# Kernel optimization log

Measured on AMD Instinct MI355X. Metric: run time of the kernel, lower is better.

Reference implementation:

```python
import jax, jax.numpy as jnp
import numpy as np

B, N_PER, N_TOOL, D, T = 64, 4096, 1000, 128, 50
SCALE = 50.0  # self.scale_pcl_val


def setup_inputs() -> dict:
    key = jax.random.key(0)
    ks = jax.random.split(key, 9)
    return {
        "x_feat": jax.random.normal(ks[0], (B * N_PER, D), jnp.float32),
        "pos": jax.random.normal(ks[1], (B * N_PER, 3), jnp.float32),
        "tool_idx": jax.random.randint(ks[2], (B, N_TOOL), 0, N_PER, jnp.int32),
        "W1": jax.random.normal(ks[3], (D, D), jnp.float32) * 0.05,
        "b1": jnp.zeros((D,), jnp.float32),
        "W2": jax.random.normal(ks[4], (D, D), jnp.float32) * 0.05,
        "b2": jnp.zeros((D,), jnp.float32),
        "W3": jax.random.normal(ks[5], (D, 3 * T), jnp.float32) * 0.05,
        "b3": jnp.zeros((3 * T,), jnp.float32),
    }


def _kabsch(xyz, flow):
    # xyz, flow: [B, N, 3]; fit rigid transform mapping xyz -> xyz + flow (Kabsch/SVD)
    y = xyz + flow
    mu_x = xyz.mean(axis=1, keepdims=True)
    mu_y = y.mean(axis=1, keepdims=True)
    xc = xyz - mu_x
    yc = y - mu_y
    H = jnp.einsum('bni,bnj->bij', xc, yc)  # [B,3,3] covariance
    U, S, Vt = jnp.linalg.svd(H)
    d = jnp.sign(jnp.linalg.det(U @ Vt))  # reflection fix, [B]
    Dm = jnp.stack([jnp.ones_like(d), jnp.ones_like(d), d], axis=-1)  # [B,3]
    R = (U * Dm[:, None, :]) @ Vt  # [B,3,3]
    return jnp.einsum('bni,bij->bnj', xc, R) + mu_y  # transformed points


def reference(x_feat, pos, tool_idx, W1, b1, W2, b2, W3, b3):
    # MLP([128,128,128,flow_dim]) head (eval mode: dropout off)
    h = jax.nn.relu(x_feat @ W1 + b1)
    h = jax.nn.relu(h @ W2 + b2)
    flow_per_pt = (h @ W3 + b3).reshape(B, N_PER, T, 3)

    pos_s = (pos * SCALE).reshape(B, N_PER, 3)  # data['pos'] * scale_pcl_val
    idx3 = tool_idx[:, :, None]
    xyz0 = jnp.take_along_axis(pos_s, idx3, axis=1)  # [B, N_TOOL, 3]
    flows = jnp.take_along_axis(flow_per_pt, tool_idx[:, :, None, None], axis=1)  # [B, N_TOOL, T, 3]
    flows_t = jnp.moveaxis(flows, 2, 0)  # [T, B, N_TOOL, 3]

    def step(xyz, flow):
        new_xyz = _kabsch(xyz, flow)
        return new_xyz, (new_xyz - xyz, flow)

    _, (flow_traj, before_svd) = jax.lax.scan(step, xyz0, flows_t)
    flow_traj = jnp.moveaxis(flow_traj, 0, 1)      # [B, T, N_TOOL, 3]
    before_svd = jnp.moveaxis(before_svd, 0, 1)    # [B, T, N_TOOL, 3]
    return flow_traj, before_svd
```

## Files before the change

kernel.cpp:

```cpp
#include <hip/hip_runtime.h>
#include <cstddef>

#define HB 64
#define HN_PER 4096
#define HN_TOOL 1000
#define HD 128
#define HT 50
#define HSCALE 50.0f

typedef _Float16 f16x8 __attribute__((ext_vector_type(8)));
typedef float f32x4 __attribute__((ext_vector_type(4)));

constexpr int TILE_M = 64;
constexpr int NBLK1 = (HB * HN_TOOL) / TILE_M;
constexpr int APITCH = 136;

constexpr int W1_BASE = 0;
constexpr int W2_BASE = 16384;
constexpr int W3_BASE = 32768;

constexpr int XC0_F = 26624;
constexpr int C0_F  = XC0_F + HB * HN_TOOL * 3;
constexpr int BT_F  = C0_F + HB * 9;
constexpr int MT_F  = BT_F + HB * HT * 12;

__global__ __launch_bounds__(256) void wconv_kernel(
    const float* __restrict__ W1, const float* __restrict__ W2,
    const float* __restrict__ W3, _Float16* __restrict__ ws)
{
    const int gid = blockIdx.x * 256 + threadIdx.x;
    const int lane = gid & 63, f = gid >> 6;
    const float* W; int ncols, base, fi;
    if (f < 32)       { W = W1; ncols = 128; base = W1_BASE; fi = f; }
    else if (f < 64)  { W = W2; ncols = 128; base = W2_BASE; fi = f - 32; }
    else if (f < 104) { W = W3; ncols = 150; base = W3_BASE; fi = f - 64; }
    else return;
    const int nt = fi >> 2, kc = fi & 3;
    const int col = nt * 16 + (lane & 15);
    const int k0 = kc * 32 + (lane >> 4) * 8;
    f16x8 v;
#pragma unroll
    for (int j = 0; j < 8; ++j)
        v[j] = (col < ncols) ? (_Float16)W[(size_t)(k0 + j) * ncols + col]
                             : (_Float16)0.f;
    *(f16x8*)(ws + ((size_t)(base + (fi * 64 + lane) * 8))) = v;
}

__device__ __forceinline__ float wave_red_sum(float v)
{
#define DPP_ADD(ctrl)                                                          \
    v += __builtin_bit_cast(float, __builtin_amdgcn_update_dpp(                \
             0, __builtin_bit_cast(int, v), (ctrl), 0xF, 0xF, true));
    DPP_ADD(0x128)
    DPP_ADD(0x124)
    DPP_ADD(0x122)
    DPP_ADD(0x121)
#undef DPP_ADD
    v += __shfl_xor(v, 16, 64);
    v += __shfl_xor(v, 32, 64);
    return v;
}

__global__ __launch_bounds__(256) void init_kernel(
    const float* __restrict__ pos,
    const int* __restrict__ tool_idx,
    float* __restrict__ ws)
{
    __shared__ float red[4][6];
    const int b = blockIdx.x;
    const int tid = threadIdx.x;
    const int lane = tid & 63, wv = tid >> 6;

    float px[4], py[4], pz[4];
    int cnt = 0;
#pragma unroll
    for (int s = 0; s < 4; ++s) {
        const int n = tid + 256 * s;
        if (n < HN_TOOL) {
            const int p = tool_idx[b * HN_TOOL + n];
            const float* pp = pos + (size_t)(b * HN_PER + p) * 3;
            px[s] = pp[0] * HSCALE;
            py[s] = pp[1] * HSCALE;
            pz[s] = pp[2] * HSCALE;
            cnt = s + 1;
        }
    }
    float s0 = 0.f, s1 = 0.f, s2 = 0.f;
    for (int s = 0; s < cnt; ++s) { s0 += px[s]; s1 += py[s]; s2 += pz[s]; }
    s0 = wave_red_sum(s0); s1 = wave_red_sum(s1); s2 = wave_red_sum(s2);
    if (lane == 0) { red[wv][0] = s0; red[wv][1] = s1; red[wv][2] = s2; }
    __syncthreads();
    const float invN = 1.0f / HN_TOOL;
    const float mux = (red[0][0] + red[1][0] + red[2][0] + red[3][0]) * invN;
    const float muy = (red[0][1] + red[1][1] + red[2][1] + red[3][1]) * invN;
    const float muz = (red[0][2] + red[1][2] + red[2][2] + red[3][2]) * invN;
    __syncthreads();

    float xx = 0.f, xy = 0.f, xz = 0.f, yy = 0.f, yz = 0.f, zz = 0.f;
    float* xc = ws + XC0_F + (size_t)b * HN_TOOL * 3;
    for (int s = 0; s < cnt; ++s) {
        const int n = tid + 256 * s;
        const float x = px[s] - mux, y = py[s] - muy, z = pz[s] - muz;
        xc[3 * n + 0] = x; xc[3 * n + 1] = y; xc[3 * n + 2] = z;
        xx += x * x; xy += x * y; xz += x * z;
        yy += y * y; yz += y * z; zz += z * z;
    }
    float c6[6] = {xx, xy, xz, yy, yz, zz};
#pragma unroll
    for (int v = 0; v < 6; ++v) c6[v] = wave_red_sum(c6[v]);
    if (lane == 0) {
#pragma unroll
        for (int v = 0; v < 6; ++v) red[wv][v] = c6[v];
    }
    __syncthreads();
    if (tid == 0) {
        float g[6];
#pragma unroll
        for (int v = 0; v < 6; ++v)
            g[v] = red[0][v] + red[1][v] + red[2][v] + red[3][v];
        float* c0 = ws + C0_F + b * 9;
        c0[0] = g[0]; c0[1] = g[1]; c0[2] = g[2];
        c0[3] = g[1]; c0[4] = g[3]; c0[5] = g[4];
        c0[6] = g[2]; c0[7] = g[4]; c0[8] = g[5];
    }
}

__global__ __launch_bounds__(256) void mlp_mfma_kernel(
    const float* __restrict__ x_feat,
    const int* __restrict__ tool_idx,
    const _Float16* __restrict__ Wsw,
    const float* __restrict__ b1, const float* __restrict__ b2,
    const float* __restrict__ b3,
    float* __restrict__ out2)
{
    __shared__ __align__(16) _Float16 hA[TILE_M][APITCH];
    const int tid = threadIdx.x;
    const int lane = tid & 63, w = tid >> 6;
    const int lm = lane & 15, quad = lane >> 4;
    const int m0 = w * 16;

    {
        const int i = tid >> 2;
        const int c0 = (tid & 3) * 32;
        const int r = blockIdx.x * TILE_M + i;
        const int b = r / HN_TOOL;
        const int n = r - b * HN_TOOL;
        const int p = tool_idx[b * HN_TOOL + n];
        const float4* src =
            (const float4*)(x_feat + (size_t)(b * HN_PER + p) * HD + c0);
#pragma unroll
        for (int fq = 0; fq < 4; ++fq) {
            const float4 u = src[2 * fq], v = src[2 * fq + 1];
            f16x8 h = {(_Float16)u.x, (_Float16)u.y, (_Float16)u.z, (_Float16)u.w,
                       (_Float16)v.x, (_Float16)v.y, (_Float16)v.z, (_Float16)v.w};
            *(f16x8*)&hA[i][c0 + fq * 8] = h;
        }
    }
    __syncthreads();

#pragma unroll
    for (int layer = 0; layer < 2; ++layer) {
        const _Float16* wb = Wsw + (layer ? W2_BASE : W1_BASE);
        const float* bias = layer ? b2 : b1;
        f16x8 afr[4];
#pragma unroll
        for (int kc = 0; kc < 4; ++kc)
            afr[kc] = *(const f16x8*)&hA[m0 + lm][kc * 32 + quad * 8];
        f32x4 acc[8];
#pragma unroll
        for (int nt = 0; nt < 8; ++nt) acc[nt] = (f32x4){0.f, 0.f, 0.f, 0.f};
#pragma unroll
        for (int kc = 0; kc < 4; ++kc)
#pragma unroll
            for (int nt = 0; nt < 8; ++nt) {
                const f16x8 bf = *(const f16x8*)(wb + (size_t)((nt * 4 + kc) * 64 + lane) * 8);
                acc[nt] = __builtin_amdgcn_mfma_f32_16x16x32_f16(afr[kc], bf, acc[nt], 0, 0, 0);
            }
#pragma unroll
        for (int nt = 0; nt < 8; ++nt) {
            const float bb = bias[nt * 16 + lm];
#pragma unroll
            for (int r = 0; r < 4; ++r)
                hA[m0 + quad * 4 + r][nt * 16 + lm] =
                    (_Float16)fmaxf(acc[nt][r] + bb, 0.f);
        }
    }

    {
        f16x8 afr[4];
#pragma unroll
        for (int kc = 0; kc < 4; ++kc)
            afr[kc] = *(const f16x8*)&hA[m0 + lm][kc * 32 + quad * 8];
        f32x4 acc[10];
#pragma unroll
        for (int nt = 0; nt < 10; ++nt) acc[nt] = (f32x4){0.f, 0.f, 0.f, 0.f};
#pragma unroll
        for (int kc = 0; kc < 4; ++kc)
#pragma unroll
            for (int nt = 0; nt < 10; ++nt) {
                const f16x8 bf = *(const f16x8*)(Wsw + W3_BASE + (size_t)((nt * 4 + kc) * 64 + lane) * 8);
                acc[nt] = __builtin_amdgcn_mfma_f32_16x16x32_f16(afr[kc], bf, acc[nt], 0, 0, 0);
            }
#pragma unroll
        for (int nt = 0; nt < 10; ++nt) {
            const int j = nt * 16 + lm;
            if (j < 150) {
                const float bb = b3[j];
                const int t = j / 3, c = j - 3 * t;
#pragma unroll
                for (int r = 0; r < 4; ++r) {
                    const int gr = blockIdx.x * TILE_M + m0 + quad * 4 + r;
                    const int b = gr / HN_TOOL;
                    const int n = gr - b * HN_TOOL;
                    out2[(size_t)b * HT * HN_TOOL * 3 +
                         ((size_t)t * HN_TOOL + n) * 3 + c] = acc[nt][r] + bb;
                }
            }
        }
    }
}

__global__ __launch_bounds__(256) void mom_kernel(
    const float* __restrict__ flows,
    float* __restrict__ ws)
{
    __shared__ float red[4][12];
    const int t = blockIdx.x, b = blockIdx.y;
    const int tid = threadIdx.x;
    const int lane = tid & 63, wv = tid >> 6;

    const float* xc = ws + XC0_F + (size_t)b * HN_TOOL * 3;
    const float* f = flows + ((size_t)(b * HT + t) * HN_TOOL) * 3;

    float S[12];
#pragma unroll
    for (int v = 0; v < 12; ++v) S[v] = 0.f;
#pragma unroll
    for (int s = 0; s < 4; ++s) {
        const int n = tid + 256 * s;
        if (n < HN_TOOL) {
            const float x = xc[3 * n + 0], y = xc[3 * n + 1], z = xc[3 * n + 2];
            const float fx = f[3 * n + 0], fy = f[3 * n + 1], fz = f[3 * n + 2];
            S[0] += x * fx; S[1] += x * fy; S[2] += x * fz;
            S[3] += y * fx; S[4] += y * fy; S[5] += y * fz;
            S[6] += z * fx; S[7] += z * fy; S[8] += z * fz;
            S[9] += fx; S[10] += fy; S[11] += fz;
        }
    }
#pragma unroll
    for (int v = 0; v < 12; ++v) S[v] = wave_red_sum(S[v]);
    if (lane == 0) {
#pragma unroll
        for (int v = 0; v < 12; ++v) red[wv][v] = S[v];
    }
    __syncthreads();
    if (tid < 12)
        ws[BT_F + (size_t)(b * HT + t) * 12 + tid] =
            red[0][tid] + red[1][tid] + red[2][tid] + red[3][tid];
}

__global__ __launch_bounds__(64) void compose_kernel(float* __restrict__ ws)
{
    const int b = threadIdx.x;
    float C0[9], P[9];
#pragma unroll
    for (int v = 0; v < 9; ++v) C0[v] = ws[C0_F + b * 9 + v];
    P[0] = 1.f; P[1] = 0.f; P[2] = 0.f;
    P[3] = 0.f; P[4] = 1.f; P[5] = 0.f;
    P[6] = 0.f; P[7] = 0.f; P[8] = 1.f;

    const float invN = 1.0f / HN_TOOL;
    const float* bt = ws + BT_F + (size_t)b * HT * 12;
    float* mt = ws + MT_F + (size_t)b * HT * 12;

    float4 n0 = *(const float4*)(bt);
    float4 n1 = *(const float4*)(bt + 4);
    float4 n2 = *(const float4*)(bt + 8);

    for (int t = 0; t < HT; ++t) {
        const float Bv[12] = {n0.x, n0.y, n0.z, n0.w, n1.x, n1.y, n1.z, n1.w,
                              n2.x, n2.y, n2.z, n2.w};
        if (t + 1 < HT) {
            const float* nb = bt + (t + 1) * 12;
            n0 = *(const float4*)(nb);
            n1 = *(const float4*)(nb + 4);
            n2 = *(const float4*)(nb + 8);
        }
        float G[9];
#pragma unroll
        for (int i = 0; i < 3; ++i)
#pragma unroll
            for (int j = 0; j < 3; ++j)
                G[i * 3 + j] = C0[i * 3 + 0] * P[0 * 3 + j] +
                               C0[i * 3 + 1] * P[1 * 3 + j] +
                               C0[i * 3 + 2] * P[2 * 3 + j] + Bv[i * 3 + j];
        float X[9];
#pragma unroll
        for (int i = 0; i < 3; ++i)
#pragma unroll
            for (int j = 0; j < 3; ++j)
                X[i * 3 + j] = P[0 * 3 + i] * G[0 * 3 + j] +
                               P[1 * 3 + i] * G[1 * 3 + j] +
                               P[2 * 3 + i] * G[2 * 3 + j];
        const float scl = 3.0f / (X[0] + X[4] + X[8]);
#pragma unroll
        for (int v = 0; v < 9; ++v) X[v] *= scl;
#pragma unroll
        for (int it = 0; it < 2; ++it) {
            float C[9];
            C[0] =  (X[4] * X[8] - X[5] * X[7]);
            C[1] = -(X[3] * X[8] - X[5] * X[6]);
            C[2] =  (X[3] * X[7] - X[4] * X[6]);
            C[3] = -(X[1] * X[8] - X[2] * X[7]);
            C[4] =  (X[0] * X[8] - X[2] * X[6]);
            C[5] = -(X[0] * X[7] - X[1] * X[6]);
            C[6] =  (X[1] * X[5] - X[2] * X[4]);
            C[7] = -(X[0] * X[5] - X[2] * X[3]);
            C[8] =  (X[0] * X[4] - X[1] * X[3]);
            const float det = X[0] * C[0] + X[1] * C[1] + X[2] * C[2];
            const float rdet = 0.5f / det;
#pragma unroll
            for (int v = 0; v < 9; ++v) X[v] = 0.5f * X[v] + C[v] * rdet;
        }
        float Pn[9];
#pragma unroll
        for (int i = 0; i < 3; ++i)
#pragma unroll
            for (int j = 0; j < 3; ++j)
                Pn[i * 3 + j] = P[i * 3 + 0] * X[0 * 3 + j] +
                                P[i * 3 + 1] * X[1 * 3 + j] +
                                P[i * 3 + 2] * X[2 * 3 + j];
        float4 m0, m1, m2;
        m0.x = Pn[0] - P[0]; m0.y = Pn[1] - P[1]; m0.z = Pn[2] - P[2];
        m0.w = Pn[3] - P[3]; m1.x = Pn[4] - P[4]; m1.y = Pn[5] - P[5];
        m1.z = Pn[6] - P[6]; m1.w = Pn[7] - P[7]; m2.x = Pn[8] - P[8];
        m2.y = Bv[9] * invN; m2.z = Bv[10] * invN; m2.w = Bv[11] * invN;
        float* mo = mt + t * 12;
        *(float4*)(mo) = m0;
        *(float4*)(mo + 4) = m1;
        *(float4*)(mo + 8) = m2;
#pragma unroll
        for (int v = 0; v < 9; ++v) P[v] = Pn[v];
    }
}

__global__ __launch_bounds__(256) void apply_kernel(
    const float* __restrict__ ws, float* __restrict__ out1)
{
    __shared__ float M[12];
    const int t = blockIdx.x, b = blockIdx.y;
    const int tid = threadIdx.x;
    if (tid < 12) M[tid] = ws[MT_F + (size_t)(b * HT + t) * 12 + tid];
    __syncthreads();

    const float* xc = ws + XC0_F + (size_t)b * HN_TOOL * 3;
    float* ot = out1 + ((size_t)(b * HT + t) * HN_TOOL) * 3;
#pragma unroll
    for (int s = 0; s < 4; ++s) {
        const int n = tid + 256 * s;
        if (n < HN_TOOL) {
            const float x = xc[3 * n + 0], y = xc[3 * n + 1], z = xc[3 * n + 2];
            ot[3 * n + 0] = x * M[0] + y * M[3] + z * M[6] + M[9];
            ot[3 * n + 1] = x * M[1] + y * M[4] + z * M[7] + M[10];
            ot[3 * n + 2] = x * M[2] + y * M[5] + z * M[8] + M[11];
        }
    }
}

extern "C" void kernel_launch(void* const* d_in, const int* in_sizes, int n_in,
                              void* d_out, int out_size, void* d_ws, size_t ws_size,
                              hipStream_t stream)
{
    const float* x_feat   = (const float*)d_in[0];
    const float* pos      = (const float*)d_in[1];
    const int*   tool_idx = (const int*)d_in[2];
    const float* W1 = (const float*)d_in[3];
    const float* b1 = (const float*)d_in[4];
    const float* W2 = (const float*)d_in[5];
    const float* b2 = (const float*)d_in[6];
    const float* W3 = (const float*)d_in[7];
    const float* b3 = (const float*)d_in[8];

    float* out1 = (float*)d_out;
    float* out2 = out1 + (size_t)HB * HT * HN_TOOL * 3;
    _Float16* wsw = (_Float16*)d_ws;
    float* wsf = (float*)d_ws;

    wconv_kernel<<<26, 256, 0, stream>>>(W1, W2, W3, wsw);
    init_kernel<<<HB, 256, 0, stream>>>(pos, tool_idx, wsf);
    mlp_mfma_kernel<<<NBLK1, 256, 0, stream>>>(
        x_feat, tool_idx, wsw, b1, b2, b3, out2);
    mom_kernel<<<dim3(HT, HB), 256, 0, stream>>>(out2, wsf);
    compose_kernel<<<1, 64, 0, stream>>>(wsf);
    apply_kernel<<<dim3(HT, HB), 256, 0, stream>>>(wsf, out1);
}
```

Baseline: 298.2 us.

## Fuse moment reduction into MLP epilogue and merge prep kernels

```diff
diff --git a/kernel.cpp b/kernel.cpp
--- a/kernel.cpp
+++ b/kernel.cpp
@@ -12,8 +12,8 @@
 typedef float f32x4 __attribute__((ext_vector_type(4)));
 
 constexpr int TILE_M = 64;
-constexpr int NBLK1 = (HB * HN_TOOL) / TILE_M;
 constexpr int APITCH = 136;
+constexpr int SPITCH = 204;
 
 constexpr int W1_BASE = 0;
 constexpr int W2_BASE = 16384;
@@ -23,28 +23,6 @@
 constexpr int C0_F  = XC0_F + HB * HN_TOOL * 3;
 constexpr int BT_F  = C0_F + HB * 9;
 constexpr int MT_F  = BT_F + HB * HT * 12;
-
-__global__ __launch_bounds__(256) void wconv_kernel(
-    const float* __restrict__ W1, const float* __restrict__ W2,
-    const float* __restrict__ W3, _Float16* __restrict__ ws)
-{
-    const int gid = blockIdx.x * 256 + threadIdx.x;
-    const int lane = gid & 63, f = gid >> 6;
-    const float* W; int ncols, base, fi;
-    if (f < 32)       { W = W1; ncols = 128; base = W1_BASE; fi = f; }
-    else if (f < 64)  { W = W2; ncols = 128; base = W2_BASE; fi = f - 32; }
-    else if (f < 104) { W = W3; ncols = 150; base = W3_BASE; fi = f - 64; }
-    else return;
-    const int nt = fi >> 2, kc = fi & 3;
-    const int col = nt * 16 + (lane & 15);
-    const int k0 = kc * 32 + (lane >> 4) * 8;
-    f16x8 v;
-#pragma unroll
-    for (int j = 0; j < 8; ++j)
-        v[j] = (col < ncols) ? (_Float16)W[(size_t)(k0 + j) * ncols + col]
-                             : (_Float16)0.f;
-    *(f16x8*)(ws + ((size_t)(base + (fi * 64 + lane) * 8))) = v;
-}
 
 __device__ __forceinline__ float wave_red_sum(float v)
 {
@@ -61,67 +39,102 @@
     return v;
 }
 
-__global__ __launch_bounds__(256) void init_kernel(
+__global__ __launch_bounds__(256) void prep_kernel(
     const float* __restrict__ pos,
     const int* __restrict__ tool_idx,
-    float* __restrict__ ws)
+    const float* __restrict__ W1, const float* __restrict__ W2,
+    const float* __restrict__ W3,
+    _Float16* __restrict__ wsh, float* __restrict__ wsf)
 {
     __shared__ float red[4][6];
-    const int b = blockIdx.x;
+    const int blk = blockIdx.x;
     const int tid = threadIdx.x;
-    const int lane = tid & 63, wv = tid >> 6;
-
-    float px[4], py[4], pz[4];
-    int cnt = 0;
-#pragma unroll
-    for (int s = 0; s < 4; ++s) {
-        const int n = tid + 256 * s;
-        if (n < HN_TOOL) {
-            const int p = tool_idx[b * HN_TOOL + n];
-            const float* pp = pos + (size_t)(b * HN_PER + p) * 3;
-            px[s] = pp[0] * HSCALE;
-            py[s] = pp[1] * HSCALE;
-            pz[s] = pp[2] * HSCALE;
-            cnt = s + 1;
-        }
-    }
-    float s0 = 0.f, s1 = 0.f, s2 = 0.f;
-    for (int s = 0; s < cnt; ++s) { s0 += px[s]; s1 += py[s]; s2 += pz[s]; }
-    s0 = wave_red_sum(s0); s1 = wave_red_sum(s1); s2 = wave_red_sum(s2);
-    if (lane == 0) { red[wv][0] = s0; red[wv][1] = s1; red[wv][2] = s2; }
-    __syncthreads();
-    const float invN = 1.0f / HN_TOOL;
-    const float mux = (red[0][0] + red[1][0] + red[2][0] + red[3][0]) * invN;
-    const float muy = (red[0][1] + red[1][1] + red[2][1] + red[3][1]) * invN;
-    const float muz = (red[0][2] + red[1][2] + red[2][2] + red[3][2]) * invN;
-    __syncthreads();
-
-    float xx = 0.f, xy = 0.f, xz = 0.f, yy = 0.f, yz = 0.f, zz = 0.f;
-    float* xc = ws + XC0_F + (size_t)b * HN_TOOL * 3;
-    for (int s = 0; s < cnt; ++s) {
-        const int n = tid + 256 * s;
-        const float x = px[s] - mux, y = py[s] - muy, z = pz[s] - muz;
-        xc[3 * n + 0] = x; xc[3 * n + 1] = y; xc[3 * n + 2] = z;
-        xx += x * x; xy += x * y; xz += x * z;
-        yy += y * y; yz += y * z; zz += z * z;
-    }
-    float c6[6] = {xx, xy, xz, yy, yz, zz};
-#pragma unroll
-    for (int v = 0; v < 6; ++v) c6[v] = wave_red_sum(c6[v]);
-    if (lane == 0) {
-#pragma unroll
-        for (int v = 0; v < 6; ++v) red[wv][v] = c6[v];
-    }
-    __syncthreads();
-    if (tid == 0) {
-        float g[6];
-#pragma unroll
-        for (int v = 0; v < 6; ++v)
-            g[v] = red[0][v] + red[1][v] + red[2][v] + red[3][v];
-        float* c0 = ws + C0_F + b * 9;
-        c0[0] = g[0]; c0[1] = g[1]; c0[2] = g[2];
-        c0[3] = g[1]; c0[4] = g[3]; c0[5] = g[4];
-        c0[6] = g[2]; c0[7] = g[4]; c0[8] = g[5];
+
+    if (blk < 64) {
+        const int b = blk;
+        const int lane = tid & 63, wv = tid >> 6;
+        const int nb = tid * 4;
+        const bool act = nb < HN_TOOL;
+
+        float xv[4], yv[4], zv[4];
+        if (act) {
+            const int4 i4 = *(const int4*)(tool_idx + b * HN_TOOL + nb);
+            const int pi[4] = {i4.x, i4.y, i4.z, i4.w};
+#pragma unroll
+            for (int s = 0; s < 4; ++s) {
+                const float* pp = pos + (size_t)(b * HN_PER + pi[s]) * 3;
+                xv[s] = pp[0] * HSCALE;
+                yv[s] = pp[1] * HSCALE;
+                zv[s] = pp[2] * HSCALE;
+            }
+        }
+        float s0 = 0.f, s1 = 0.f, s2 = 0.f;
+        if (act) {
+#pragma unroll
+            for (int s = 0; s < 4; ++s) { s0 += xv[s]; s1 += yv[s]; s2 += zv[s]; }
+        }
+        s0 = wave_red_sum(s0); s1 = wave_red_sum(s1); s2 = wave_red_sum(s2);
+        if (lane == 0) { red[wv][0] = s0; red[wv][1] = s1; red[wv][2] = s2; }
+        __syncthreads();
+        const float invN = 1.0f / HN_TOOL;
+        const float mux = (red[0][0] + red[1][0] + red[2][0] + red[3][0]) * invN;
+        const float muy = (red[0][1] + red[1][1] + red[2][1] + red[3][1]) * invN;
+        const float muz = (red[0][2] + red[1][2] + red[2][2] + red[3][2]) * invN;
+        __syncthreads();
+
+        float xx = 0.f, xy = 0.f, xz = 0.f, yy = 0.f, yz = 0.f, zz = 0.f;
+        if (act) {
+            float o[12];
+#pragma unroll
+            for (int s = 0; s < 4; ++s) {
+                const float x = xv[s] - mux, y = yv[s] - muy, z = zv[s] - muz;
+                o[3 * s + 0] = x; o[3 * s + 1] = y; o[3 * s + 2] = z;
+                xx += x * x; xy += x * y; xz += x * z;
+                yy += y * y; yz += y * z; zz += z * z;
+            }
+            float4* dst = (float4*)(wsf + XC0_F + (size_t)b * (HN_TOOL * 3) + nb * 3);
+            dst[0] = *(float4*)&o[0];
+            dst[1] = *(float4*)&o[4];
+            dst[2] = *(float4*)&o[8];
+        }
+        float c6[6] = {xx, xy, xz, yy, yz, zz};
+#pragma unroll
+        for (int v = 0; v < 6; ++v) c6[v] = wave_red_sum(c6[v]);
+        if (lane == 0) {
+#pragma unroll
+            for (int v = 0; v < 6; ++v) red[wv][v] = c6[v];
+        }
+        __syncthreads();
+        if (tid == 0) {
+            float g[6];
+#pragma unroll
+            for (int v = 0; v < 6; ++v)
+                g[v] = red[0][v] + red[1][v] + red[2][v] + red[3][v];
+            float* c0 = wsf + C0_F + b * 9;
+            c0[0] = g[0]; c0[1] = g[1]; c0[2] = g[2];
+            c0[3] = g[1]; c0[4] = g[3]; c0[5] = g[4];
+            c0[6] = g[2]; c0[7] = g[4]; c0[8] = g[5];
+        }
+    } else if (blk < 90) {
+        const int lane = tid & 63;
+        const int f = (blk - 64) * 4 + (tid >> 6);
+        const float* W; int ncols, base, fi;
+        if (f < 32)       { W = W1; ncols = 128; base = W1_BASE; fi = f; }
+        else if (f < 64)  { W = W2; ncols = 128; base = W2_BASE; fi = f - 32; }
+        else              { W = W3; ncols = 150; base = W3_BASE; fi = f - 64; }
+        const int nt = fi >> 2, kc = fi & 3;
+        const int col = nt * 16 + (lane & 15);
+        const int k0 = kc * 32 + (lane >> 4) * 8;
+        f16x8 v;
+#pragma unroll
+        for (int j = 0; j < 8; ++j)
+            v[j] = (col < ncols) ? (_Float16)W[(size_t)(k0 + j) * ncols + col]
+                                 : (_Float16)0.f;
+        *(f16x8*)(wsh + ((size_t)(base + (fi * 64 + lane) * 8))) = v;
+    } else {
+        const float4 z4 = {0.f, 0.f, 0.f, 0.f};
+        float4* bt4 = (float4*)(wsf + BT_F);
+        for (int i = tid; i < (HB * HT * 12) / 4; i += 256) bt4[i] = z4;
     }
 }
 
@@ -131,21 +144,26 @@
     const _Float16* __restrict__ Wsw,
     const float* __restrict__ b1, const float* __restrict__ b2,
     const float* __restrict__ b3,
-    float* __restrict__ out2)
-{
-    __shared__ __align__(16) _Float16 hA[TILE_M][APITCH];
+    float* __restrict__ out2, float* __restrict__ wsf)
+{
+    __shared__ __align__(16) char smem[HT * SPITCH * 4];
+    _Float16 (*hA)[APITCH] = (_Float16 (*)[APITCH])smem;
+    float* stage = (float*)smem;
+
     const int tid = threadIdx.x;
     const int lane = tid & 63, w = tid >> 6;
     const int lm = lane & 15, quad = lane >> 4;
     const int m0 = w * 16;
+    const int bx = blockIdx.x;
+    const int b  = blockIdx.y;
+    const int n0 = bx * TILE_M;
 
     {
         const int i = tid >> 2;
         const int c0 = (tid & 3) * 32;
-        const int r = blockIdx.x * TILE_M + i;
-        const int b = r / HN_TOOL;
-        const int n = r - b * HN_TOOL;
-        const int p = tool_idx[b * HN_TOOL + n];
+        const int n = n0 + i;
+        const int nc = (n < HN_TOOL) ? n : (HN_TOOL - 1);
+        const int p = tool_idx[b * HN_TOOL + nc];
         const float4* src =
             (const float4*)(x_feat + (size_t)(b * HN_PER + p) * HD + c0);
 #pragma unroll
@@ -191,6 +209,7 @@
 #pragma unroll
         for (int kc = 0; kc < 4; ++kc)
             afr[kc] = *(const f16x8*)&hA[m0 + lm][kc * 32 + quad * 8];
+        __syncthreads();
         f32x4 acc[10];
 #pragma unroll
         for (int nt = 0; nt < 10; ++nt) acc[nt] = (f32x4){0.f, 0.f, 0.f, 0.f};
@@ -208,55 +227,57 @@
                 const float bb = b3[j];
                 const int t = j / 3, c = j - 3 * t;
 #pragma unroll
-                for (int r = 0; r < 4; ++r) {
-                    const int gr = blockIdx.x * TILE_M + m0 + quad * 4 + r;
-                    const int b = gr / HN_TOOL;
-                    const int n = gr - b * HN_TOOL;
-                    out2[(size_t)b * HT * HN_TOOL * 3 +
-                         ((size_t)t * HN_TOOL + n) * 3 + c] = acc[nt][r] + bb;
-                }
-            }
-        }
-    }
-}
-
-__global__ __launch_bounds__(256) void mom_kernel(
-    const float* __restrict__ flows,
-    float* __restrict__ ws)
-{
-    __shared__ float red[4][12];
-    const int t = blockIdx.x, b = blockIdx.y;
-    const int tid = threadIdx.x;
-    const int lane = tid & 63, wv = tid >> 6;
-
-    const float* xc = ws + XC0_F + (size_t)b * HN_TOOL * 3;
-    const float* f = flows + ((size_t)(b * HT + t) * HN_TOOL) * 3;
-
-    float S[12];
-#pragma unroll
-    for (int v = 0; v < 12; ++v) S[v] = 0.f;
-#pragma unroll
-    for (int s = 0; s < 4; ++s) {
-        const int n = tid + 256 * s;
-        if (n < HN_TOOL) {
-            const float x = xc[3 * n + 0], y = xc[3 * n + 1], z = xc[3 * n + 2];
-            const float fx = f[3 * n + 0], fy = f[3 * n + 1], fz = f[3 * n + 2];
-            S[0] += x * fx; S[1] += x * fy; S[2] += x * fz;
-            S[3] += y * fx; S[4] += y * fy; S[5] += y * fz;
-            S[6] += z * fx; S[7] += z * fy; S[8] += z * fz;
-            S[9] += fx; S[10] += fy; S[11] += fz;
-        }
-    }
-#pragma unroll
-    for (int v = 0; v < 12; ++v) S[v] = wave_red_sum(S[v]);
-    if (lane == 0) {
-#pragma unroll
-        for (int v = 0; v < 12; ++v) red[wv][v] = S[v];
+                for (int r = 0; r < 4; ++r)
+                    stage[t * SPITCH + (m0 + quad * 4 + r) * 3 + c] = acc[nt][r] + bb;
+            }
+        }
     }
     __syncthreads();
-    if (tid < 12)
-        ws[BT_F + (size_t)(b * HT + t) * 12 + tid] =
-            red[0][tid] + red[1][tid] + red[2][tid] + red[3][tid];
+
+    const int V = (bx == 15) ? (HN_TOOL - 15 * TILE_M) : TILE_M;
+    const int nf4 = (V * 3) >> 2;
+    {
+        float* ob = out2 + (size_t)b * HT * (HN_TOOL * 3) + (size_t)n0 * 3;
+        for (int t = w; t < HT; t += 4) {
+            if (lane < nf4) {
+                const f32x4 v = *(const f32x4*)&stage[t * SPITCH + lane * 4];
+                __builtin_nontemporal_store(
+                    v, (f32x4*)(ob + (size_t)t * (HN_TOOL * 3)) + lane);
+            }
+        }
+    }
+
+    if (tid < 4 * HT) {
+        const int t = tid >> 2, part = tid & 3;
+        const float* xc = wsf + XC0_F + (size_t)b * (HN_TOOL * 3) + (size_t)n0 * 3;
+        float S[12];
+#pragma unroll
+        for (int v = 0; v < 12; ++v) S[v] = 0.f;
+#pragma unroll
+        for (int rr = 0; rr < 16; ++rr) {
+            const int nl = part * 16 + rr;
+            if (n0 + nl < HN_TOOL) {
+                const float x = xc[3 * nl + 0], y = xc[3 * nl + 1], z = xc[3 * nl + 2];
+                const float fx = stage[t * SPITCH + 3 * nl + 0];
+                const float fy = stage[t * SPITCH + 3 * nl + 1];
+                const float fz = stage[t * SPITCH + 3 * nl + 2];
+                S[0] += x * fx; S[1] += x * fy; S[2] += x * fz;
+                S[3] += y * fx; S[4] += y * fy; S[5] += y * fz;
+                S[6] += z * fx; S[7] += z * fy; S[8] += z * fz;
+                S[9] += fx; S[10] += fy; S[11] += fz;
+            }
+        }
+#pragma unroll
+        for (int v = 0; v < 12; ++v) {
+            S[v] += __shfl_xor(S[v], 1, 64);
+            S[v] += __shfl_xor(S[v], 2, 64);
+        }
+        if (part == 0) {
+            float* btp = wsf + BT_F + ((size_t)b * HT + t) * 12;
+#pragma unroll
+            for (int v = 0; v < 12; ++v) atomicAdd(btp + v, S[v]);
+        }
+    }
 }
 
 __global__ __launch_bounds__(64) void compose_kernel(float* __restrict__ ws)
@@ -302,7 +323,7 @@
                 X[i * 3 + j] = P[0 * 3 + i] * G[0 * 3 + j] +
                                P[1 * 3 + i] * G[1 * 3 + j] +
                                P[2 * 3 + i] * G[2 * 3 + j];
-        const float scl = 3.0f / (X[0] + X[4] + X[8]);
+        const float scl = 3.0f * __builtin_amdgcn_rcpf(X[0] + X[4] + X[8]);
 #pragma unroll
         for (int v = 0; v < 9; ++v) X[v] *= scl;
 #pragma unroll
@@ -318,7 +339,7 @@
             C[7] = -(X[0] * X[5] - X[2] * X[3]);
             C[8] =  (X[0] * X[4] - X[1] * X[3]);
             const float det = X[0] * C[0] + X[1] * C[1] + X[2] * C[2];
-            const float rdet = 0.5f / det;
+            const float rdet = 0.5f * __builtin_amdgcn_rcpf(det);
 #pragma unroll
             for (int v = 0; v < 9; ++v) X[v] = 0.5f * X[v] + C[v] * rdet;
         }
@@ -353,17 +374,25 @@
     if (tid < 12) M[tid] = ws[MT_F + (size_t)(b * HT + t) * 12 + tid];
     __syncthreads();
 
-    const float* xc = ws + XC0_F + (size_t)b * HN_TOOL * 3;
-    float* ot = out1 + ((size_t)(b * HT + t) * HN_TOOL) * 3;
-#pragma unroll
-    for (int s = 0; s < 4; ++s) {
-        const int n = tid + 256 * s;
-        if (n < HN_TOOL) {
-            const float x = xc[3 * n + 0], y = xc[3 * n + 1], z = xc[3 * n + 2];
-            ot[3 * n + 0] = x * M[0] + y * M[3] + z * M[6] + M[9];
-            ot[3 * n + 1] = x * M[1] + y * M[4] + z * M[7] + M[10];
-            ot[3 * n + 2] = x * M[2] + y * M[5] + z * M[8] + M[11];
-        }
+    const int nb = tid * 4;
+    if (nb < HN_TOOL) {
+        const float4* xc4 =
+            (const float4*)(ws + XC0_F + (size_t)b * (HN_TOOL * 3) + nb * 3);
+        float in12[12], o12[12];
+        *(float4*)&in12[0] = xc4[0];
+        *(float4*)&in12[4] = xc4[1];
+        *(float4*)&in12[8] = xc4[2];
+#pragma unroll
+        for (int k = 0; k < 4; ++k) {
+            const float x = in12[3 * k], y = in12[3 * k + 1], z = in12[3 * k + 2];
+            o12[3 * k + 0] = x * M[0] + y * M[3] + z * M[6] + M[9];
+            o12[3 * k + 1] = x * M[1] + y * M[4] + z * M[7] + M[10];
+            o12[3 * k + 2] = x * M[2] + y * M[5] + z * M[8] + M[11];
+        }
+        f32x4* ot = (f32x4*)(out1 + ((size_t)(b * HT + t) * HN_TOOL) * 3 + nb * 3);
+        __builtin_nontemporal_store(*(f32x4*)&o12[0], ot + 0);
+        __builtin_nontemporal_store(*(f32x4*)&o12[4], ot + 1);
+        __builtin_nontemporal_store(*(f32x4*)&o12[8], ot + 2);
     }
 }
 
@@ -386,11 +415,9 @@
     _Float16* wsw = (_Float16*)d_ws;
     float* wsf = (float*)d_ws;
 
-    wconv_kernel<<<26, 256, 0, stream>>>(W1, W2, W3, wsw);
-    init_kernel<<<HB, 256, 0, stream>>>(pos, tool_idx, wsf);
-    mlp_mfma_kernel<<<NBLK1, 256, 0, stream>>>(
-        x_feat, tool_idx, wsw, b1, b2, b3, out2);
-    mom_kernel<<<dim3(HT, HB), 256, 0, stream>>>(out2, wsf);
+    prep_kernel<<<91, 256, 0, stream>>>(pos, tool_idx, W1, W2, W3, wsw, wsf);
+    mlp_mfma_kernel<<<dim3(16, HB), 256, 0, stream>>>(
+        x_feat, tool_idx, wsw, b1, b2, b3, out2, wsf);
     compose_kernel<<<1, 64, 0, stream>>>(wsf);
     apply_kernel<<<dim3(HT, HB), 256, 0, stream>>>(wsf, out1);
 }
```

Result: slower. 330.7 us (+10.9%).
